# Performance work log

Measured on AMD Instinct MI355X. Metric: run time of the kernel, lower is better.

Reference implementation:

```python
import jax, jax.numpy as jnp
import numpy as np


def setup_inputs() -> dict:
    key = jax.random.key(0)
    k1, k2 = jax.random.split(key)
    T, H, E = 16384, 4096, 8
    x = jax.random.normal(k1, (T, H), dtype=jnp.float32)
    W = jax.random.normal(k2, (E, H), dtype=jnp.float32) * 0.02  # torch Linear weight [out, in]
    return {"x": x, "W": W, "top_k": 2}


def reference(x, W, top_k):
    # router_logits = x @ W^T : [T, E]
    logits = jnp.einsum("th,eh->te", x, W)
    scores = jax.nn.softmax(logits.astype(jnp.float32), axis=-1)
    expert_weights, expert_indices = jax.lax.top_k(scores, top_k)
    return scores, expert_weights, expert_indices.astype(jnp.int32)
```

## Files before the change

kernel.cpp:

```cpp
#include <hip/hip_runtime.h>


#define ROUTER_H 4096
#define ROUTER_E 8
#define ROWS_PER_WAVE 4

__global__ __launch_bounds__(256) void learned_router_kernel(
    const float* __restrict__ x, const float* __restrict__ W,
    float* __restrict__ out_scores, float* __restrict__ out_w,
    float* __restrict__ out_idx, int n_rows)
{
    const int wave = (int)((blockIdx.x * blockDim.x + threadIdx.x) >> 6);
    const int lane = (int)(threadIdx.x & 63);
    const int row0 = wave * ROWS_PER_WAVE;
    if (row0 >= n_rows) return;

    const float4* __restrict__ x4 = (const float4*)x;
    const float4* __restrict__ W4 = (const float4*)W;

    float acc[ROWS_PER_WAVE][ROUTER_E];
#pragma unroll
    for (int r = 0; r < ROWS_PER_WAVE; ++r)
#pragma unroll
        for (int e = 0; e < ROUTER_E; ++e) acc[r][e] = 0.f;

#pragma unroll 2
    for (int j = 0; j < (ROUTER_H / 4) / 64; ++j) {
        const int idx = j * 64 + lane;
        float4 xv[ROWS_PER_WAVE];
#pragma unroll
        for (int r = 0; r < ROWS_PER_WAVE; ++r)
            xv[r] = x4[(size_t)(row0 + r) * (ROUTER_H / 4) + idx];
#pragma unroll
        for (int e = 0; e < ROUTER_E; ++e) {
            const float4 wv = W4[e * (ROUTER_H / 4) + idx];
#pragma unroll
            for (int r = 0; r < ROWS_PER_WAVE; ++r)
                acc[r][e] += xv[r].x * wv.x + xv[r].y * wv.y
                           + xv[r].z * wv.z + xv[r].w * wv.w;
        }
    }

#pragma unroll
    for (int off = 32; off > 0; off >>= 1) {
#pragma unroll
        for (int r = 0; r < ROWS_PER_WAVE; ++r)
#pragma unroll
            for (int e = 0; e < ROUTER_E; ++e)
                acc[r][e] += __shfl_xor(acc[r][e], off, 64);
    }

    if (lane == 0) {
#pragma unroll
        for (int r = 0; r < ROWS_PER_WAVE; ++r) {
            const int row = row0 + r;
            float m = acc[r][0];
#pragma unroll
            for (int e = 1; e < ROUTER_E; ++e) m = fmaxf(m, acc[r][e]);
            float p[ROUTER_E];
            float s = 0.f;
#pragma unroll
            for (int e = 0; e < ROUTER_E; ++e) { p[e] = __expf(acc[r][e] - m); s += p[e]; }
            const float inv = 1.f / s;
#pragma unroll
            for (int e = 0; e < ROUTER_E; ++e) p[e] *= inv;

            float4* os = (float4*)(out_scores + (size_t)row * ROUTER_E);
            os[0] = make_float4(p[0], p[1], p[2], p[3]);
            os[1] = make_float4(p[4], p[5], p[6], p[7]);

            int i0 = 0;
#pragma unroll
            for (int e = 1; e < ROUTER_E; ++e) if (p[e] > p[i0]) i0 = e;
            int i1 = (i0 == 0) ? 1 : 0;
#pragma unroll
            for (int e = 0; e < ROUTER_E; ++e) if (e != i0 && p[e] > p[i1]) i1 = e;

            *(float2*)(out_w + (size_t)row * 2)   = make_float2(p[i0], p[i1]);
            *(float2*)(out_idx + (size_t)row * 2) = make_float2((float)i0, (float)i1);
        }
    }
}

extern "C" void kernel_launch(void* const* d_in, const int* in_sizes, int n_in,
                              void* d_out, int out_size, void* d_ws, size_t ws_size,
                              hipStream_t stream) {
    const float* x = (const float*)d_in[0];
    const float* W = (const float*)d_in[1];
    const int T = in_sizes[0] / ROUTER_H;
    (void)n_in; (void)d_ws; (void)ws_size; (void)out_size;

    float* out = (float*)d_out;
    float* out_scores = out;
    float* out_w   = out + (size_t)T * ROUTER_E;
    float* out_idx = out_w + (size_t)T * 2;

    const int rows_per_block = 4 * ROWS_PER_WAVE;
    const int grid = (T + rows_per_block - 1) / rows_per_block;
    learned_router_kernel<<<grid, 256, 0, stream>>>(x, W, out_scores, out_w, out_idx, T);
}
```

Baseline: 367.5 us.

## Stage router weight chunks in shared memory with larger 512-thread blocks

Loads chunks of the expert weight matrix cooperatively into LDS once per block and has each wave read weights from LDS instead of global/cache for every row group. Block size grows to 512 threads (8 waves, 32 rows) so each staged chunk is reused across more rows. This is meant to cut repeated L1/L2 weight traffic, at the cost of two barriers per chunk, 32KB of LDS per block, and removal of the out-of-range row guard.

```diff
diff --git a/kernel.cpp b/kernel.cpp
--- a/kernel.cpp
+++ b/kernel.cpp
@@ -1,19 +1,23 @@
 #include <hip/hip_runtime.h>
 
 
-#define ROUTER_H 4096
+#define ROUTER_H4 1024
 #define ROUTER_E 8
 #define ROWS_PER_WAVE 4
+#define CHUNK 256
+#define NCHUNK (ROUTER_H4 / CHUNK)
 
-__global__ __launch_bounds__(256) void learned_router_kernel(
+__global__ __launch_bounds__(512, 4) void learned_router_kernel(
     const float* __restrict__ x, const float* __restrict__ W,
     float* __restrict__ out_scores, float* __restrict__ out_w,
     float* __restrict__ out_idx, int n_rows)
 {
-    const int wave = (int)((blockIdx.x * blockDim.x + threadIdx.x) >> 6);
-    const int lane = (int)(threadIdx.x & 63);
-    const int row0 = wave * ROWS_PER_WAVE;
-    if (row0 >= n_rows) return;
+    __shared__ float4 wlds[ROUTER_E][CHUNK];
+
+    const int tid  = (int)threadIdx.x;
+    const int wv   = tid >> 6;
+    const int lane = tid & 63;
+    const int row0 = (int)blockIdx.x * (8 * ROWS_PER_WAVE) + wv * ROWS_PER_WAVE;
 
     const float4* __restrict__ x4 = (const float4*)x;
     const float4* __restrict__ W4 = (const float4*)W;
@@ -24,21 +28,33 @@
 #pragma unroll
         for (int e = 0; e < ROUTER_E; ++e) acc[r][e] = 0.f;
 
-#pragma unroll 2
-    for (int j = 0; j < (ROUTER_H / 4) / 64; ++j) {
-        const int idx = j * 64 + lane;
-        float4 xv[ROWS_PER_WAVE];
+    for (int c = 0; c < NCHUNK; ++c) {
 #pragma unroll
-        for (int r = 0; r < ROWS_PER_WAVE; ++r)
-            xv[r] = x4[(size_t)(row0 + r) * (ROUTER_H / 4) + idx];
+        for (int k = 0; k < 4; ++k) {
+            const int flat = k * 512 + tid;
+            const int e    = flat >> 8;
+            const int pos  = flat & (CHUNK - 1);
+            wlds[e][pos] = W4[e * ROUTER_H4 + c * CHUNK + pos];
+        }
+        __syncthreads();
+
 #pragma unroll
-        for (int e = 0; e < ROUTER_E; ++e) {
-            const float4 wv = W4[e * (ROUTER_H / 4) + idx];
+        for (int inner = 0; inner < CHUNK / 64; ++inner) {
+            const int hpos = c * CHUNK + inner * 64 + lane;
+            float4 xv[ROWS_PER_WAVE];
 #pragma unroll
             for (int r = 0; r < ROWS_PER_WAVE; ++r)
-                acc[r][e] += xv[r].x * wv.x + xv[r].y * wv.y
-                           + xv[r].z * wv.z + xv[r].w * wv.w;
+                xv[r] = x4[(size_t)(row0 + r) * ROUTER_H4 + hpos];
+#pragma unroll
+            for (int e = 0; e < ROUTER_E; ++e) {
+                const float4 w4 = wlds[e][inner * 64 + lane];
+#pragma unroll
+                for (int r = 0; r < ROWS_PER_WAVE; ++r)
+                    acc[r][e] += xv[r].x * w4.x + xv[r].y * w4.y
+                               + xv[r].z * w4.z + xv[r].w * w4.w;
+            }
         }
+        __syncthreads();
     }
 
 #pragma unroll
@@ -87,7 +103,7 @@
                               hipStream_t stream) {
     const float* x = (const float*)d_in[0];
     const float* W = (const float*)d_in[1];
-    const int T = in_sizes[0] / ROUTER_H;
+    const int T = in_sizes[0] / (ROUTER_H4 * 4);
     (void)n_in; (void)d_ws; (void)ws_size; (void)out_size;
 
     float* out = (float*)d_out;
@@ -95,7 +111,7 @@
     float* out_w   = out + (size_t)T * ROUTER_E;
     float* out_idx = out_w + (size_t)T * 2;
 
-    const int rows_per_block = 4 * ROWS_PER_WAVE;
+    const int rows_per_block = 8 * ROWS_PER_WAVE;
     const int grid = (T + rows_per_block - 1) / rows_per_block;
-    learned_router_kernel<<<grid, 256, 0, stream>>>(x, W, out_scores, out_w, out_idx, T);
+    learned_router_kernel<<<grid, 512, 0, stream>>>(x, W, out_scores, out_w, out_idx, T);
 }
```

Result: slower. 464.5 us (+26.4%).
